# Kernel optimization log

Measured on AMD Instinct MI355X. Metric: run time of the kernel, lower is better.

Reference implementation:

```python
import jax, jax.numpy as jnp
import numpy as np

D = 1024
H = 16
FF = 4 * D


def layer_norm(x, g, b, eps=1e-5):
    mu = jnp.mean(x, axis=-1, keepdims=True)
    var = jnp.var(x, axis=-1, keepdims=True)
    return (x - mu) * jax.lax.rsqrt(var + eps) * g + b


def setup_inputs() -> dict:
    key = jax.random.key(0)
    ks = jax.random.split(key, 8)
    s = lambda fan_in: 1.0 / np.sqrt(fan_in)
    return {
        "x": jax.random.normal(ks[0], (2, 2048, D), dtype=jnp.float32),
        "ln1_g": jnp.ones((D,), jnp.float32),
        "ln1_b": jnp.zeros((D,), jnp.float32),
        "w_qkv": jax.random.uniform(ks[1], (D, 3 * D), jnp.float32, -s(D), s(D)),
        "b_qkv": jnp.zeros((3 * D,), jnp.float32),
        "w_out": jax.random.uniform(ks[2], (D, D), jnp.float32, -s(D), s(D)),
        "b_out": jnp.zeros((D,), jnp.float32),
        "ln2_g": jnp.ones((D,), jnp.float32),
        "ln2_b": jnp.zeros((D,), jnp.float32),
        "w_fc1": jax.random.uniform(ks[3], (D, FF), jnp.float32, -s(D), s(D)),
        "b_fc1": jnp.zeros((FF,), jnp.float32),
        "w_fc2": jax.random.uniform(ks[4], (FF, D), jnp.float32, -s(FF), s(FF)),
        "b_fc2": jnp.zeros((D,), jnp.float32),
    }


def reference(x, ln1_g, ln1_b, w_qkv, b_qkv, w_out, b_out,
              ln2_g, ln2_b, w_fc1, b_fc1, w_fc2, b_fc2):
    b, n, c = x.shape
    hd = c // H
    scale = hd ** -0.5

    # --- pre-norm MHA ---
    h = layer_norm(x, ln1_g, ln1_b)
    qkv = h @ w_qkv + b_qkv                      # [b,n,3c]
    qkv = qkv.reshape(b, n, 3, H, hd)
    q = jnp.transpose(qkv[:, :, 0], (0, 2, 1, 3))  # [b,H,n,hd]
    k = jnp.transpose(qkv[:, :, 1], (0, 2, 1, 3))
    v = jnp.transpose(qkv[:, :, 2], (0, 2, 1, 3))
    attn = jnp.einsum('bhqd,bhkd->bhqk', q, k) * scale
    attn = jax.nn.softmax(attn, axis=-1)
    o = jnp.einsum('bhqk,bhkd->bhqd', attn, v)   # [b,H,n,hd]
    o = jnp.transpose(o, (0, 2, 1, 3)).reshape(b, n, c)
    x = x + (o @ w_out + b_out)

    # --- pre-norm FFN ---
    h = layer_norm(x, ln2_g, ln2_b)
    h = jax.nn.gelu(h @ w_fc1 + b_fc1, approximate=False)
    x = x + (h @ w_fc2 + b_fc2)
    return x
```

## Files before the change

kernel.cpp:

```cpp
#include <hip/hip_runtime.h>
#include <stdint.h>
#include <math.h>

#define D_MODEL 1024
#define NHEAD   16
#define HDIM    64
#define FFDIM   4096
#define SEQ     2048
#define BATCH   2
#define NTOK    (BATCH*SEQ)
#define QKVN    (3*D_MODEL)

typedef __bf16 bf16;
typedef __attribute__((ext_vector_type(8))) __bf16 bf16x8;
typedef __attribute__((ext_vector_type(4))) __bf16 bf16x4;
typedef __attribute__((ext_vector_type(4))) float f32x4;

__device__ __forceinline__ void gld_lds16(const void* g, void* l) {
    __builtin_amdgcn_global_load_lds((__attribute__((address_space(1))) void*)g,
                                     (__attribute__((address_space(3))) void*)l,
                                     16, 0, 0);
}

__device__ __forceinline__ float fast_exp2(float x) {
#if __has_builtin(__builtin_amdgcn_exp2f)
    return __builtin_amdgcn_exp2f(x);
#else
    return __expf(x * 0.69314718056f);
#endif
}

__device__ __forceinline__ float fast_rcp(float x) {
#if __has_builtin(__builtin_amdgcn_rcpf)
    return __builtin_amdgcn_rcpf(x);
#else
    return 1.0f / x;
#endif
}

__device__ __forceinline__ float gelu_fast(float x) {
    float xx = x * x;
    float y  = x * fmaf(0.035677408137f, xx, 0.7978845608f);
    float z  = fminf(-2.8853900817779268f * y, 126.0f);
    float e  = fast_exp2(z);
    return x * fast_rcp(1.0f + e);
}

#define GEMM_BAR() do {                                        \
    asm volatile("s_waitcnt lgkmcnt(0)" ::: "memory");         \
    __builtin_amdgcn_s_barrier();                              \
    asm volatile("" ::: "memory");                             \
} while (0)

__global__ __launch_bounds__(256)
void k_transpose_all(const float* __restrict__ w_qkv, const float* __restrict__ w_out,
                     const float* __restrict__ w_fc1, const float* __restrict__ w_fc2,
                     bf16* __restrict__ t_qkv, bf16* __restrict__ t_out,
                     bf16* __restrict__ t_fc1, bf16* __restrict__ t_fc2) {
    __shared__ float tile[32][33];
    int bid = blockIdx.x;
    const float* W; bf16* Wt; int K, N, ti;
    if (bid < 3072)       { W = w_qkv; Wt = t_qkv; K = 1024; N = 3072; ti = bid; }
    else if (bid < 4096)  { W = w_out; Wt = t_out; K = 1024; N = 1024; ti = bid - 3072; }
    else if (bid < 8192)  { W = w_fc1; Wt = t_fc1; K = 1024; N = 4096; ti = bid - 4096; }
    else                  { W = w_fc2; Wt = t_fc2; K = 4096; N = 1024; ti = bid - 8192; }
    int tn = N >> 5;
    int n0 = (ti % tn) * 32, k0 = (ti / tn) * 32;
    int tx = threadIdx.x, ty = threadIdx.y;
#pragma unroll
    for (int i = 0; i < 4; i++)
        tile[ty + i * 8][tx] = W[(size_t)(k0 + ty + i * 8) * N + n0 + tx];
    __syncthreads();
#pragma unroll
    for (int i = 0; i < 4; i++)
        Wt[(size_t)(n0 + ty + i * 8) * K + k0 + tx] = (bf16)tile[tx][ty + i * 8];
}

__global__ __launch_bounds__(256)
void k_vtrans(const bf16* __restrict__ qkv, bf16* __restrict__ vT) {
    __shared__ bf16 t[32][33];
    int tok0 = blockIdx.x * 32, f0 = blockIdx.y * 32;
    int tx = threadIdx.x, ty = threadIdx.y;
#pragma unroll
    for (int i = 0; i < 4; i++)
        t[ty + i * 8][tx] = qkv[(size_t)(tok0 + ty + i * 8) * QKVN + 2 * D_MODEL + f0 + tx];
    __syncthreads();
    int s = tx;
    int pp = (s < 16) ? ((s >> 2) * 8 + (s & 3))
                      : (((s - 16) >> 2) * 8 + ((s - 16) & 3) + 4);
#pragma unroll
    for (int i = 0; i < 4; i++)
        vT[(size_t)(f0 + ty + i * 8) * NTOK + tok0 + pp] = t[tx][ty + i * 8];
}

__global__ __launch_bounds__(256)
void k_layernorm(const float* __restrict__ x, const float* __restrict__ g,
                 const float* __restrict__ b, bf16* __restrict__ out) {
    int row = blockIdx.x;
    int tid = threadIdx.x;
    float4 v = ((const float4*)(x + (size_t)row * D_MODEL))[tid];
    float s  = v.x + v.y + v.z + v.w;
    float ss = v.x * v.x + v.y * v.y + v.z * v.z + v.w * v.w;
#pragma unroll
    for (int off = 32; off > 0; off >>= 1) {
        s  += __shfl_down(s, off, 64);
        ss += __shfl_down(ss, off, 64);
    }
    __shared__ float red[2][4];
    __shared__ float mv[2];
    int wave = tid >> 6, lane = tid & 63;
    if (lane == 0) { red[0][wave] = s; red[1][wave] = ss; }
    __syncthreads();
    if (tid == 0) {
        float S  = red[0][0] + red[0][1] + red[0][2] + red[0][3];
        float SS = red[1][0] + red[1][1] + red[1][2] + red[1][3];
        float mu = S * (1.0f / D_MODEL);
        float var = SS * (1.0f / D_MODEL) - mu * mu;
        mv[0] = mu;
        mv[1] = rsqrtf(var + 1e-5f);
    }
    __syncthreads();
    float mu = mv[0], rs = mv[1];
    float4 gv = ((const float4*)g)[tid];
    float4 bv = ((const float4*)b)[tid];
    bf16x4 ov = { (bf16)((v.x - mu) * rs * gv.x + bv.x),
                  (bf16)((v.y - mu) * rs * gv.y + bv.y),
                  (bf16)((v.z - mu) * rs * gv.z + bv.z),
                  (bf16)((v.w - mu) * rs * gv.w + bv.w) };
    *(bf16x4*)(out + (size_t)row * D_MODEL + tid * 4) = ov;
}

template <int DO_GELU, int DO_RES, int OUT_BF16, int BN, int PIPE2, int SPLITK, int STAGE>
__global__ __launch_bounds__(256)
void k_gemm(const bf16* __restrict__ A, const bf16* __restrict__ Bt,
            const float* __restrict__ bias, const float* __restrict__ res,
            float* __restrict__ outf, bf16* __restrict__ outb,
            float* __restrict__ part, int M, int N, int K) {
    constexpr int WN = BN / 32;
    constexpr int NBUF = STAGE ? 1 : 2;
    __shared__ bf16 As[NBUF][128 * 32];
    __shared__ bf16 Bs[NBUF][BN * 32];
    int tid  = threadIdx.x;
    int wave = tid >> 6, lane = tid & 63;
    int quad = lane >> 4, l16 = lane & 15;

    int nwg = gridDim.x * gridDim.y;
    int bid = blockIdx.y * gridDim.x + blockIdx.x;
    int sid = (bid & 7) * (nwg >> 3) + (bid >> 3);
    int bx = sid % gridDim.x, by = sid / gridDim.x;
    int m0 = by * 128, n0 = bx * BN;
    int wm = (wave >> 1) * 64, wn = (wave & 1) * (BN / 2);

    int Keff = (SPLITK == 2) ? (K >> 1) : K;
    int koff = (SPLITK == 2) ? blockIdx.z * Keff : 0;

    f32x4 acc[4][WN];
#pragma unroll
    for (int i = 0; i < 4; i++)
#pragma unroll
        for (int j = 0; j < WN; j++) acc[i][j] = (f32x4){0.f, 0.f, 0.f, 0.f};

    int lrow = lane >> 2;
    int lcol = (lane & 3) * 8;
    const bf16* gA0 = A + (size_t)(m0 + wave * 32 + lrow) * K + koff + lcol;
    const bf16* gA1 = gA0 + (size_t)16 * K;
    const bf16* gB0;
    const bf16* gB1 = nullptr;
    if constexpr (BN == 128) {
        gB0 = Bt + (size_t)(n0 + wave * 32 + lrow) * K + koff + lcol;
        gB1 = gB0 + (size_t)16 * K;
    } else {
        gB0 = Bt + (size_t)(n0 + wave * 16 + lrow) * K + koff + lcol;
    }

    int wA0 = wave * 1024 + lane * 8;
    int wA1 = wA0 + 512;
    int wB0 = (BN == 128) ? (wave * 1024 + lane * 8) : (wave * 512 + lane * 8);
    int wB1 = wB0 + 512;

    auto issue = [&](bf16x8* r, int k0) {
        r[0] = *(const bf16x8*)(gA0 + k0);
        r[1] = *(const bf16x8*)(gA1 + k0);
        r[2] = *(const bf16x8*)(gB0 + k0);
        if constexpr (BN == 128) r[3] = *(const bf16x8*)(gB1 + k0);
    };
    auto commit = [&](int buf, const bf16x8* r) {
        *(bf16x8*)(&As[buf][wA0]) = r[0];
        *(bf16x8*)(&As[buf][wA1]) = r[1];
        *(bf16x8*)(&Bs[buf][wB0]) = r[2];
        if constexpr (BN == 128) *(bf16x8*)(&Bs[buf][wB1]) = r[3];
    };
    auto compute = [&](int buf) {
        bf16x8 af[4], bfr[WN];
#pragma unroll
        for (int mi = 0; mi < 4; mi++)
            af[mi] = *(const bf16x8*)(&As[buf][(wm + mi * 16 + l16) * 32 + quad * 8]);
#pragma unroll
        for (int ni = 0; ni < WN; ni++)
            bfr[ni] = *(const bf16x8*)(&Bs[buf][(wn + ni * 16 + l16) * 32 + quad * 8]);
#pragma unroll
        for (int mi = 0; mi < 4; mi++)
#pragma unroll
            for (int ni = 0; ni < WN; ni++)
                acc[mi][ni] = __builtin_amdgcn_mfma_f32_16x16x32_bf16(af[mi], bfr[ni], acc[mi][ni], 0, 0, 0);
    };

    int niter = Keff / 32;

    if constexpr (STAGE == 1) {
        bf16* lA0 = &As[0][wave * 1024];
        bf16* lA1 = lA0 + 512;
        bf16* lB0 = &Bs[0][(BN == 128) ? wave * 1024 : wave * 512];
        bf16* lB1 = lB0 + 512;
        for (int t = 0; t < niter; t++) {
            int k0 = t * 32;
            __syncthreads();
            gld_lds16(gA0 + k0, lA0);
            gld_lds16(gA1 + k0, lA1);
            gld_lds16(gB0 + k0, lB0);
            if constexpr (BN == 128) gld_lds16(gB1 + k0, lB1);
            __syncthreads();
            compute(0);
        }
    } else if constexpr (!PIPE2) {
        bf16x8 r0[4];
        issue(r0, 0);
        commit(0, r0);
        __syncthreads();
        for (int t = 1; t < niter; t++) {
            issue(r0, t * 32);
            compute((t - 1) & 1);
            commit(t & 1, r0);
            __syncthreads();
        }
        compute((niter - 1) & 1);
    } else {
        bf16x8 r0[4], r1[4];
        issue(r0, 0);
        commit(0, r0);
        issue(r1, 32);
        GEMM_BAR();
        for (int t = 1; t + 2 < niter; t += 2) {
            issue(r0, (t + 1) * 32);
            compute(0);
            commit(1, r1);
            GEMM_BAR();
            issue(r1, (t + 2) * 32);
            compute(1);
            commit(0, r0);
            GEMM_BAR();
        }
        compute(0);
        commit(1, r1);
        GEMM_BAR();
        compute(1);
    }

#pragma unroll
    for (int mi = 0; mi < 4; mi++) {
        int row = m0 + wm + mi * 16 + quad * 4;
#pragma unroll
        for (int ni = 0; ni < WN; ni++) {
            int col = n0 + wn + ni * 16 + l16;
            if constexpr (SPLITK == 2) {
                if (blockIdx.z == 1) {
#pragma unroll
                    for (int r = 0; r < 4; r++)
                        part[(size_t)(row + r) * N + col] = acc[mi][ni][r];
                    continue;
                }
            }
            float bb = bias[col];
#pragma unroll
            for (int r = 0; r < 4; r++) {
                float v = acc[mi][ni][r] + bb;
                if (DO_GELU) v = gelu_fast(v);
                size_t idx = (size_t)(row + r) * N + col;
                if (DO_RES) v += res[idx];
                if (OUT_BF16) outb[idx] = (bf16)v;
                else          outf[idx] = v;
            }
        }
    }
}

__global__ __launch_bounds__(256)
void k_add(float* __restrict__ out, const float* __restrict__ part) {
    size_t i = (size_t)blockIdx.x * 256 + threadIdx.x;
    float4* o = (float4*)out;
    const float4* p = (const float4*)part;
    float4 a = o[i], q = p[i];
    a.x += q.x; a.y += q.y; a.z += q.z; a.w += q.w;
    o[i] = a;
}

__global__ __launch_bounds__(256)
void k_attention2(const bf16* __restrict__ qkv, const bf16* __restrict__ vT,
                  bf16* __restrict__ o) {
    __shared__ bf16 Ks[2][64][32];
    __shared__ bf16 Vs[2][64][32];

    int tid = threadIdx.x, wave = tid >> 6, lane = tid & 63;
    int quad = lane >> 4, l16 = lane & 15;
    int bh = blockIdx.y;
    int b = bh >> 4, h = bh & 15;
    int q0 = blockIdx.x * 64 + wave * 16;

    const bf16* Qb  = qkv + (size_t)b * SEQ * QKVN + h * HDIM;
    const bf16* Kb  = Qb + D_MODEL;
    const bf16* vTb = vT + (size_t)h * HDIM * NTOK + b * SEQ;

    const float QSCALE = 0.125f * 1.44269504089f;
    bf16x8 qf[2];
#pragma unroll
    for (int c = 0; c < 2; c++) {
        bf16x8 qraw = *(const bf16x8*)(Qb + (size_t)(q0 + l16) * QKVN + c * 32 + quad * 8);
#pragma unroll
        for (int i = 0; i < 8; i++) qf[c][i] = (bf16)((float)qraw[i] * QSCALE);
    }

    const bf16* gK0 = Kb + (size_t)(wave * 16 + (lane >> 2)) * QKVN + 0 * 32 + (lane & 3) * 8;
    const bf16* gK1 = gK0 + 32;
    const bf16* gV0 = vTb + (size_t)(wave * 16 + (lane >> 2)) * NTOK + (lane & 3) * 8;
    const bf16* gV1 = gV0 + 32;
    bf16* lK0 = &Ks[0][wave * 16][0];
    bf16* lK1 = &Ks[1][wave * 16][0];
    bf16* lV0 = &Vs[0][wave * 16][0];
    bf16* lV1 = &Vs[1][wave * 16][0];

    f32x4 oacc[4];
#pragma unroll
    for (int i = 0; i < 4; i++) oacc[i] = (f32x4){0.f, 0.f, 0.f, 0.f};
    float lsum = 0.f;

    for (int kv0 = 0; kv0 < SEQ; kv0 += 64) {
        __syncthreads();
        size_t koff = (size_t)kv0 * QKVN;
        gld_lds16(gK0 + koff, lK0);
        gld_lds16(gK1 + koff, lK1);
        gld_lds16(gV0 + kv0, lV0);
        gld_lds16(gV1 + kv0, lV1);
        __syncthreads();

        f32x4 s[4];
#pragma unroll
        for (int t = 0; t < 4; t++) {
            bf16x8 af0 = *(const bf16x8*)(&Ks[0][t * 16 + l16][quad * 8]);
            bf16x8 af1 = *(const bf16x8*)(&Ks[1][t * 16 + l16][quad * 8]);
            f32x4 z = (f32x4){0.f, 0.f, 0.f, 0.f};
            z = __builtin_amdgcn_mfma_f32_16x16x32_bf16(af0, qf[0], z, 0, 0, 0);
            z = __builtin_amdgcn_mfma_f32_16x16x32_bf16(af1, qf[1], z, 0, 0, 0);
            s[t] = z;
        }

        bf16x4 p[4];
#pragma unroll
        for (int t = 0; t < 4; t++)
#pragma unroll
            for (int r = 0; r < 4; r++) {
                float pf = fast_exp2(s[t][r]);
                lsum += pf;
                p[t][r] = (bf16)pf;
            }

#pragma unroll
        for (int tp = 0; tp < 2; tp++) {
            bf16x8 pa = __builtin_shufflevector(p[2 * tp], p[2 * tp + 1], 0, 1, 2, 3, 4, 5, 6, 7);
#pragma unroll
            for (int nt = 0; nt < 4; nt++) {
                bf16x8 vb = *(const bf16x8*)(&Vs[tp][nt * 16 + l16][quad * 8]);
                oacc[nt] = __builtin_amdgcn_mfma_f32_16x16x32_bf16(pa, vb, oacc[nt], 0, 0, 0);
            }
        }
    }

    lsum += __shfl_xor(lsum, 16, 64);
    lsum += __shfl_xor(lsum, 32, 64);
    float invl[4];
#pragma unroll
    for (int r = 0; r < 4; r++)
        invl[r] = 1.0f / __shfl(lsum, quad * 4 + r, 16);

#pragma unroll
    for (int nt = 0; nt < 4; nt++)
#pragma unroll
        for (int r = 0; r < 4; r++)
            o[(size_t)(b * SEQ + q0 + quad * 4 + r) * D_MODEL + h * HDIM + nt * 16 + l16] =
                (bf16)(oacc[nt][r] * invl[r]);
}

extern "C" void kernel_launch(void* const* d_in, const int* in_sizes, int n_in,
                              void* d_out, int out_size, void* d_ws, size_t ws_size,
                              hipStream_t stream) {
    const float* x     = (const float*)d_in[0];
    const float* ln1_g = (const float*)d_in[1];
    const float* ln1_b = (const float*)d_in[2];
    const float* w_qkv = (const float*)d_in[3];
    const float* b_qkv = (const float*)d_in[4];
    const float* w_out = (const float*)d_in[5];
    const float* b_out = (const float*)d_in[6];
    const float* ln2_g = (const float*)d_in[7];
    const float* ln2_b = (const float*)d_in[8];
    const float* w_fc1 = (const float*)d_in[9];
    const float* b_fc1 = (const float*)d_in[10];
    const float* w_fc2 = (const float*)d_in[11];
    const float* b_fc2 = (const float*)d_in[12];
    float* out = (float*)d_out;

    uintptr_t ws = (uintptr_t)d_ws;
    bf16* wt_qkv = (bf16*)(ws + 0);
    bf16* wt_out = (bf16*)(ws + 6291456);
    bf16* wt_fc1 = (bf16*)(ws + 8388608);
    bf16* wt_fc2 = (bf16*)(ws + 16777216);
    bf16* hbuf   = (bf16*)(ws + 25165824);
    bf16* vT     = hbuf;
    bf16* qkv    = (bf16*)(ws + 33554432);
    bf16* attn_o = (bf16*)(ws + 58720256);
    bf16* hgelu  = (bf16*)(ws + 33554432);
    float* fc2p  = (float*)(ws + 0);

    k_transpose_all<<<12288, dim3(32, 8), 0, stream>>>(w_qkv, w_out, w_fc1, w_fc2,
                                                       wt_qkv, wt_out, wt_fc1, wt_fc2);

    k_layernorm<<<NTOK, 256, 0, stream>>>(x, ln1_g, ln1_b, hbuf);

    k_gemm<0, 0, 1, 128, 0, 1, 1><<<dim3(QKVN / 128, NTOK / 128), 256, 0, stream>>>(
        hbuf, wt_qkv, b_qkv, nullptr, nullptr, qkv, nullptr, NTOK, QKVN, D_MODEL);

    k_vtrans<<<dim3(NTOK / 32, D_MODEL / 32), dim3(32, 8), 0, stream>>>(qkv, vT);

    k_attention2<<<dim3(SEQ / 64, BATCH * NHEAD), 256, 0, stream>>>(qkv, vT, attn_o);

    k_gemm<0, 1, 0, 64, 1, 1, 0><<<dim3(D_MODEL / 64, NTOK / 128), 256, 0, stream>>>(
        attn_o, wt_out, b_out, x, out, nullptr, nullptr, NTOK, D_MODEL, D_MODEL);

    k_layernorm<<<NTOK, 256, 0, stream>>>(out, ln2_g, ln2_b, hbuf);

    k_gemm<1, 0, 1, 128, 0, 1, 1><<<dim3(FFDIM / 128, NTOK / 128), 256, 0, stream>>>(
        hbuf, wt_fc1, b_fc1, nullptr, nullptr, hgelu, nullptr, NTOK, FFDIM, D_MODEL);

    k_gemm<0, 1, 0, 128, 1, 2, 0><<<dim3(D_MODEL / 128, NTOK / 128, 2), 256, 0, stream>>>(
        hgelu, wt_fc2, b_fc2, out, out, nullptr, fc2p, NTOK, D_MODEL, FFDIM);

    k_add<<<(NTOK * D_MODEL / 4) / 256, 256, 0, stream>>>(out, fc2p);
}
```

Measured before the change: 365.3 us.

## Double-buffer direct-to-LDS loads in GEMM and attention; atomic split-K reduction

```diff
diff --git a/kernel.cpp b/kernel.cpp
--- a/kernel.cpp
+++ b/kernel.cpp
@@ -45,6 +45,12 @@
     float e  = fast_exp2(z);
     return x * fast_rcp(1.0f + e);
 }
+
+#define PHASE_BAR() do {                                       \
+    asm volatile("s_waitcnt vmcnt(0)" ::: "memory");           \
+    __builtin_amdgcn_s_barrier();                              \
+    asm volatile("" ::: "memory");                             \
+} while (0)
 
 #define GEMM_BAR() do {                                        \
     asm volatile("s_waitcnt lgkmcnt(0)" ::: "memory");         \
@@ -135,11 +141,10 @@
 void k_gemm(const bf16* __restrict__ A, const bf16* __restrict__ Bt,
             const float* __restrict__ bias, const float* __restrict__ res,
             float* __restrict__ outf, bf16* __restrict__ outb,
-            float* __restrict__ part, int M, int N, int K) {
+            int M, int N, int K) {
     constexpr int WN = BN / 32;
-    constexpr int NBUF = STAGE ? 1 : 2;
-    __shared__ bf16 As[NBUF][128 * 32];
-    __shared__ bf16 Bs[NBUF][BN * 32];
+    __shared__ bf16 As[2][128 * 32];
+    __shared__ bf16 Bs[2][BN * 32];
     int tid  = threadIdx.x;
     int wave = tid >> 6, lane = tid & 63;
     int quad = lane >> 4, l16 = lane & 15;
@@ -190,14 +195,14 @@
         *(bf16x8*)(&Bs[buf][wB0]) = r[2];
         if constexpr (BN == 128) *(bf16x8*)(&Bs[buf][wB1]) = r[3];
     };
-    auto compute = [&](int buf) {
+    auto compute = [&](const bf16* cA, const bf16* cB) {
         bf16x8 af[4], bfr[WN];
 #pragma unroll
         for (int mi = 0; mi < 4; mi++)
-            af[mi] = *(const bf16x8*)(&As[buf][(wm + mi * 16 + l16) * 32 + quad * 8]);
+            af[mi] = *(const bf16x8*)(cA + (wm + mi * 16 + l16) * 32 + quad * 8);
 #pragma unroll
         for (int ni = 0; ni < WN; ni++)
-            bfr[ni] = *(const bf16x8*)(&Bs[buf][(wn + ni * 16 + l16) * 32 + quad * 8]);
+            bfr[ni] = *(const bf16x8*)(cB + (wn + ni * 16 + l16) * 32 + quad * 8);
 #pragma unroll
         for (int mi = 0; mi < 4; mi++)
 #pragma unroll
@@ -208,20 +213,31 @@
     int niter = Keff / 32;
 
     if constexpr (STAGE == 1) {
-        bf16* lA0 = &As[0][wave * 1024];
-        bf16* lA1 = lA0 + 512;
-        bf16* lB0 = &Bs[0][(BN == 128) ? wave * 1024 : wave * 512];
-        bf16* lB1 = lB0 + 512;
-        for (int t = 0; t < niter; t++) {
+        bf16* sA  = &As[0][wave * 1024];
+        bf16* sB  = &Bs[0][(BN == 128) ? wave * 1024 : wave * 512];
+        bf16* sA2 = &As[1][wave * 1024];
+        bf16* sB2 = &Bs[1][(BN == 128) ? wave * 1024 : wave * 512];
+        const bf16* rA  = &As[0][0]; const bf16* rB  = &Bs[0][0];
+        const bf16* rA2 = &As[1][0]; const bf16* rB2 = &Bs[1][0];
+        gld_lds16(gA0, sA);
+        gld_lds16(gA1, sA + 512);
+        gld_lds16(gB0, sB);
+        if constexpr (BN == 128) gld_lds16(gB1, sB + 512);
+        PHASE_BAR();
+        for (int t = 1; t < niter; t++) {
             int k0 = t * 32;
-            __syncthreads();
-            gld_lds16(gA0 + k0, lA0);
-            gld_lds16(gA1 + k0, lA1);
-            gld_lds16(gB0 + k0, lB0);
-            if constexpr (BN == 128) gld_lds16(gB1 + k0, lB1);
-            __syncthreads();
-            compute(0);
-        }
+            gld_lds16(gA0 + k0, sA2);
+            gld_lds16(gA1 + k0, sA2 + 512);
+            gld_lds16(gB0 + k0, sB2);
+            if constexpr (BN == 128) gld_lds16(gB1 + k0, sB2 + 512);
+            compute(rA, rB);
+            PHASE_BAR();
+            bf16* t0 = sA; sA = sA2; sA2 = t0;
+            bf16* t1 = sB; sB = sB2; sB2 = t1;
+            const bf16* t2 = rA; rA = rA2; rA2 = t2;
+            const bf16* t3 = rB; rB = rB2; rB2 = t3;
+        }
+        compute(rA, rB);
     } else if constexpr (!PIPE2) {
         bf16x8 r0[4];
         issue(r0, 0);
@@ -229,11 +245,11 @@
         __syncthreads();
         for (int t = 1; t < niter; t++) {
             issue(r0, t * 32);
-            compute((t - 1) & 1);
+            compute(&As[(t - 1) & 1][0], &Bs[(t - 1) & 1][0]);
             commit(t & 1, r0);
             __syncthreads();
         }
-        compute((niter - 1) & 1);
+        compute(&As[(niter - 1) & 1][0], &Bs[(niter - 1) & 1][0]);
     } else {
         bf16x8 r0[4], r1[4];
         issue(r0, 0);
@@ -242,18 +258,18 @@
         GEMM_BAR();
         for (int t = 1; t + 2 < niter; t += 2) {
             issue(r0, (t + 1) * 32);
-            compute(0);
+            compute(&As[0][0], &Bs[0][0]);
             commit(1, r1);
             GEMM_BAR();
             issue(r1, (t + 2) * 32);
-            compute(1);
+            compute(&As[1][0], &Bs[1][0]);
             commit(0, r0);
             GEMM_BAR();
         }
-        compute(0);
+        compute(&As[0][0], &Bs[0][0]);
         commit(1, r1);
         GEMM_BAR();
-        compute(1);
+        compute(&As[1][0], &Bs[1][0]);
     }
 
 #pragma unroll
@@ -263,12 +279,11 @@
         for (int ni = 0; ni < WN; ni++) {
             int col = n0 + wn + ni * 16 + l16;
             if constexpr (SPLITK == 2) {
-                if (blockIdx.z == 1) {
-#pragma unroll
-                    for (int r = 0; r < 4; r++)
-                        part[(size_t)(row + r) * N + col] = acc[mi][ni][r];
-                    continue;
-                }
+                float bb = (blockIdx.z == 0) ? bias[col] : 0.0f;
+#pragma unroll
+                for (int r = 0; r < 4; r++)
+                    atomicAdd(&outf[(size_t)(row + r) * N + col], acc[mi][ni][r] + bb);
+                continue;
             }
             float bb = bias[col];
 #pragma unroll
@@ -285,20 +300,10 @@
 }
 
 __global__ __launch_bounds__(256)
-void k_add(float* __restrict__ out, const float* __restrict__ part) {
-    size_t i = (size_t)blockIdx.x * 256 + threadIdx.x;
-    float4* o = (float4*)out;
-    const float4* p = (const float4*)part;
-    float4 a = o[i], q = p[i];
-    a.x += q.x; a.y += q.y; a.z += q.z; a.w += q.w;
-    o[i] = a;
-}
-
-__global__ __launch_bounds__(256)
 void k_attention2(const bf16* __restrict__ qkv, const bf16* __restrict__ vT,
                   bf16* __restrict__ o) {
-    __shared__ bf16 Ks[2][64][32];
-    __shared__ bf16 Vs[2][64][32];
+    __shared__ bf16 Ks[2][2][64][32];
+    __shared__ bf16 Vs[2][2][64][32];
 
     int tid = threadIdx.x, wave = tid >> 6, lane = tid & 63;
     int quad = lane >> 4, l16 = lane & 15;
@@ -319,34 +324,39 @@
         for (int i = 0; i < 8; i++) qf[c][i] = (bf16)((float)qraw[i] * QSCALE);
     }
 
-    const bf16* gK0 = Kb + (size_t)(wave * 16 + (lane >> 2)) * QKVN + 0 * 32 + (lane & 3) * 8;
+    const bf16* gK0 = Kb + (size_t)(wave * 16 + (lane >> 2)) * QKVN + (lane & 3) * 8;
     const bf16* gK1 = gK0 + 32;
     const bf16* gV0 = vTb + (size_t)(wave * 16 + (lane >> 2)) * NTOK + (lane & 3) * 8;
     const bf16* gV1 = gV0 + 32;
-    bf16* lK0 = &Ks[0][wave * 16][0];
-    bf16* lK1 = &Ks[1][wave * 16][0];
-    bf16* lV0 = &Vs[0][wave * 16][0];
-    bf16* lV1 = &Vs[1][wave * 16][0];
 
     f32x4 oacc[4];
 #pragma unroll
     for (int i = 0; i < 4; i++) oacc[i] = (f32x4){0.f, 0.f, 0.f, 0.f};
     float lsum = 0.f;
 
+    {
+        gld_lds16(gK0, &Ks[0][0][wave * 16][0]);
+        gld_lds16(gK1, &Ks[0][1][wave * 16][0]);
+        gld_lds16(gV0, &Vs[0][0][wave * 16][0]);
+        gld_lds16(gV1, &Vs[0][1][wave * 16][0]);
+    }
+    PHASE_BAR();
+
+    int buf = 0;
     for (int kv0 = 0; kv0 < SEQ; kv0 += 64) {
-        __syncthreads();
-        size_t koff = (size_t)kv0 * QKVN;
-        gld_lds16(gK0 + koff, lK0);
-        gld_lds16(gK1 + koff, lK1);
-        gld_lds16(gV0 + kv0, lV0);
-        gld_lds16(gV1 + kv0, lV1);
-        __syncthreads();
+        if (kv0 + 64 < SEQ) {
+            size_t koff = (size_t)(kv0 + 64) * QKVN;
+            gld_lds16(gK0 + koff, &Ks[buf ^ 1][0][wave * 16][0]);
+            gld_lds16(gK1 + koff, &Ks[buf ^ 1][1][wave * 16][0]);
+            gld_lds16(gV0 + kv0 + 64, &Vs[buf ^ 1][0][wave * 16][0]);
+            gld_lds16(gV1 + kv0 + 64, &Vs[buf ^ 1][1][wave * 16][0]);
+        }
 
         f32x4 s[4];
 #pragma unroll
         for (int t = 0; t < 4; t++) {
-            bf16x8 af0 = *(const bf16x8*)(&Ks[0][t * 16 + l16][quad * 8]);
-            bf16x8 af1 = *(const bf16x8*)(&Ks[1][t * 16 + l16][quad * 8]);
+            bf16x8 af0 = *(const bf16x8*)(&Ks[buf][0][t * 16 + l16][quad * 8]);
+            bf16x8 af1 = *(const bf16x8*)(&Ks[buf][1][t * 16 + l16][quad * 8]);
             f32x4 z = (f32x4){0.f, 0.f, 0.f, 0.f};
             z = __builtin_amdgcn_mfma_f32_16x16x32_bf16(af0, qf[0], z, 0, 0, 0);
             z = __builtin_amdgcn_mfma_f32_16x16x32_bf16(af1, qf[1], z, 0, 0, 0);
@@ -368,10 +378,13 @@
             bf16x8 pa = __builtin_shufflevector(p[2 * tp], p[2 * tp + 1], 0, 1, 2, 3, 4, 5, 6, 7);
 #pragma unroll
             for (int nt = 0; nt < 4; nt++) {
-                bf16x8 vb = *(const bf16x8*)(&Vs[tp][nt * 16 + l16][quad * 8]);
+                bf16x8 vb = *(const bf16x8*)(&Vs[buf][tp][nt * 16 + l16][quad * 8]);
                 oacc[nt] = __builtin_amdgcn_mfma_f32_16x16x32_bf16(pa, vb, oacc[nt], 0, 0, 0);
             }
         }
+
+        PHASE_BAR();
+        buf ^= 1;
     }
 
     lsum += __shfl_xor(lsum, 16, 64);
@@ -417,7 +430,6 @@
     bf16* qkv    = (bf16*)(ws + 33554432);
     bf16* attn_o = (bf16*)(ws + 58720256);
     bf16* hgelu  = (bf16*)(ws + 33554432);
-    float* fc2p  = (float*)(ws + 0);
 
     k_transpose_all<<<12288, dim3(32, 8), 0, stream>>>(w_qkv, w_out, w_fc1, w_fc2,
                                                        wt_qkv, wt_out, wt_fc1, wt_fc2);
@@ -425,22 +437,20 @@
     k_layernorm<<<NTOK, 256, 0, stream>>>(x, ln1_g, ln1_b, hbuf);
 
     k_gemm<0, 0, 1, 128, 0, 1, 1><<<dim3(QKVN / 128, NTOK / 128), 256, 0, stream>>>(
-        hbuf, wt_qkv, b_qkv, nullptr, nullptr, qkv, nullptr, NTOK, QKVN, D_MODEL);
+        hbuf, wt_qkv, b_qkv, nullptr, nullptr, qkv, NTOK, QKVN, D_MODEL);
 
     k_vtrans<<<dim3(NTOK / 32, D_MODEL / 32), dim3(32, 8), 0, stream>>>(qkv, vT);
 
     k_attention2<<<dim3(SEQ / 64, BATCH * NHEAD), 256, 0, stream>>>(qkv, vT, attn_o);
 
     k_gemm<0, 1, 0, 64, 1, 1, 0><<<dim3(D_MODEL / 64, NTOK / 128), 256, 0, stream>>>(
-        attn_o, wt_out, b_out, x, out, nullptr, nullptr, NTOK, D_MODEL, D_MODEL);
+        attn_o, wt_out, b_out, x, out, nullptr, NTOK, D_MODEL, D_MODEL);
 
     k_layernorm<<<NTOK, 256, 0, stream>>>(out, ln2_g, ln2_b, hbuf);
 
     k_gemm<1, 0, 1, 128, 0, 1, 1><<<dim3(FFDIM / 128, NTOK / 128), 256, 0, stream>>>(
-        hbuf, wt_fc1, b_fc1, nullptr, nullptr, hgelu, nullptr, NTOK, FFDIM, D_MODEL);
-
-    k_gemm<0, 1, 0, 128, 1, 2, 0><<<dim3(D_MODEL / 128, NTOK / 128, 2), 256, 0, stream>>>(
-        hgelu, wt_fc2, b_fc2, out, out, nullptr, fc2p, NTOK, D_MODEL, FFDIM);
-
-    k_add<<<(NTOK * D_MODEL / 4) / 256, 256, 0, stream>>>(out, fc2p);
-}
+        hbuf, wt_fc1, b_fc1, nullptr, nullptr, hgelu, NTOK, FFDIM, D_MODEL);
+
+    k_gemm<0, 0, 0, 128, 1, 2, 0><<<dim3(D_MODEL / 128, NTOK / 128, 2), 256, 0, stream>>>(
+        hgelu, wt_fc2, b_fc2, nullptr, out, nullptr, NTOK, D_MODEL, FFDIM);
+}
```

Result: no change. 358.8 us (-1.8%).
